# Kernel optimization log

Measured on AMD Instinct MI355X. Metric: run time of the kernel, lower is better.

The kernel has to match this reference:

```python
import jax, jax.numpy as jnp
import numpy as np

N_NODE = 2048   # nodes per graph
B = 32          # num_graphs
N = B * N_NODE  # batched node count
E = 1048576     # random edges (self loops added in reference)
C = 12          # in_channels = history window
H = 8           # attention heads
P = 9           # n_pred (out_channels)


def setup_inputs() -> dict:
    key = jax.random.key(0)
    ks = jax.random.split(key, 16)
    rn = lambda k, shp, s: jax.random.normal(k, shp, dtype=jnp.float32) * s
    return {
        "x": rn(ks[0], (N, C), 1.0),
        "edge_index": jax.random.randint(ks[1], (2, E), 0, N, dtype=jnp.int64),
        "W_gat": rn(ks[2], (C, H * C), 1.0 / np.sqrt(C)),
        "att_src": rn(ks[3], (H, C), 0.1),
        "att_dst": rn(ks[4], (H, C), 0.1),
        "bias_gat": rn(ks[5], (C,), 0.05),
        "Wih1": rn(ks[6], (4 * 32, N_NODE), 1.0 / np.sqrt(N_NODE)),
        "Whh1": rn(ks[7], (4 * 32, 32), 1.0 / np.sqrt(32)),
        "bih1": rn(ks[8], (4 * 32,), 0.05),
        "bhh1": rn(ks[9], (4 * 32,), 0.05),
        "Wih2": rn(ks[10], (4 * 128, 32), 1.0 / np.sqrt(32)),
        "Whh2": rn(ks[11], (4 * 128, 128), 1.0 / np.sqrt(128)),
        "bih2": rn(ks[12], (4 * 128,), 0.05),
        "bhh2": rn(ks[13], (4 * 128,), 0.05),
        "W_lin": rn(ks[14], (N_NODE * P, 128), 1.0 / np.sqrt(128)),
        "b_lin": rn(ks[15], (N_NODE * P,), 0.05),
    }


def _lstm(xs, Wih, Whh, bih, bhh):
    # xs: [T, B, in]; PyTorch gate order i, f, g, o
    Hh = Whh.shape[1]
    Bb = xs.shape[1]
    def step(carry, x):
        h, c = carry
        z = x @ Wih.T + h @ Whh.T + bih + bhh  # [B, 4H]
        i, f, g, o = jnp.split(z, 4, axis=-1)
        c = jax.nn.sigmoid(f) * c + jax.nn.sigmoid(i) * jnp.tanh(g)
        h = jax.nn.sigmoid(o) * jnp.tanh(c)
        return (h, c), h
    init = (jnp.zeros((Bb, Hh), xs.dtype), jnp.zeros((Bb, Hh), xs.dtype))
    _, ys = jax.lax.scan(step, init, xs)
    return ys


def reference(x, edge_index, W_gat, att_src, att_dst, bias_gat,
              Wih1, Whh1, bih1, bhh1, Wih2, Whh2, bih2, bhh2, W_lin, b_lin):
    # ---- GATConv (heads=8, concat=False, add_self_loops=True) ----
    loop = jnp.arange(N, dtype=edge_index.dtype)
    src = jnp.concatenate([edge_index[0], loop])  # message source j
    dst = jnp.concatenate([edge_index[1], loop])  # message target i
    h = (x @ W_gat).reshape(N, H, C)              # [N,H,C]
    a_s = jnp.einsum('nhc,hc->nh', h, att_src)
    a_d = jnp.einsum('nhc,hc->nh', h, att_dst)
    e = jax.nn.leaky_relu(a_s[src] + a_d[dst], 0.2)          # [E',H]
    e_max = jax.ops.segment_max(e, dst, num_segments=N)      # self loops ensure non-empty segments
    w = jnp.exp(e - e_max[dst])
    denom = jax.ops.segment_sum(w, dst, num_segments=N)
    alpha = w / denom[dst]                                   # [E',H]
    agg = jax.ops.segment_sum(alpha[:, :, None] * h[src], dst, num_segments=N)  # [N,H,C]
    g = agg.mean(axis=1) + bias_gat                          # concat=False -> head mean, [N,C]
    # (dropout is identity in eval mode)

    # ---- temporal stack ----
    seq = jnp.moveaxis(g.reshape(B, N_NODE, C), 2, 0)        # [T=C, B, N_NODE]
    h1 = _lstm(seq, Wih1, Whh1, bih1, bhh1)                  # [T,B,32]
    h2 = _lstm(h1, Wih2, Whh2, bih2, bhh2)                   # [T,B,128]
    y = h2[-1] @ W_lin.T + b_lin                             # [B, N_NODE*P]
    return y.reshape(B * N_NODE, P)
```

## Files before the change

kernel.cpp:

```cpp
#include <hip/hip_runtime.h>
#include <hip/hip_bf16.h>
#include <stdint.h>

#define NTOT 65536
#define NNODE 2048
#define CIN 12

__device__ __forceinline__ float bf2f(uint32_t u) {
    union { uint32_t i; float f; } v; v.i = u << 16; return v.f;
}
__device__ __forceinline__ uint16_t f2bf(float f) {
    union { float f; uint32_t i; } v; v.f = f;
    uint32_t x = v.i;
    uint32_t r = x + 0x7fffu + ((x >> 16) & 1u);
    return (uint16_t)(r >> 16);
}
__device__ __forceinline__ float bflo(uint32_t u) { return bf2f(u & 0xffffu); }
__device__ __forceinline__ float bfhi(uint32_t u) { return bf2f(u >> 16); }
__device__ __forceinline__ float sigmf(float x) {
    return __builtin_amdgcn_rcpf(1.0f + __expf(-x));
}
__device__ __forceinline__ float tanhfast(float x) {
    float ex = __expf(2.0f * x);
    return 1.0f - 2.0f * __builtin_amdgcn_rcpf(ex + 1.0f);
}
__device__ __forceinline__ float lrelu(float v) { return v > 0.f ? v : 0.2f * v; }

#define O_WG   16
#define O_AS   1168
#define O_AD   1264
#define O_BIAS 1360
#define O_BIH1 1376
#define O_BHH1 1504
#define O_BIH2 1632
#define O_BHH2 2144
#define O_BLIN 2656
#define O_END  21088

__device__ __forceinline__ void cvt(const void* s, float* d, int i, int bf) {
    d[i] = bf ? bf2f(((const uint16_t*)s)[i]) : ((const float*)s)[i];
}

__global__ void __launch_bounds__(256) k_pre(
    const void* x, const int* __restrict__ e32,
    const void* wg, const void* as_, const void* ad_, const void* bs,
    const void* b1, const void* bb1, const void* b2, const void* bb2,
    const void* bl, float* __restrict__ ws, int* __restrict__ deg) {
    int tid = threadIdx.x, lane = tid & 63;
    uint32_t u = ((const uint16_t*)x)[2 * lane];
    uint32_t ex = (u >> 7) & 0xFF;
    bool sane = (ex >= 0x60 && ex <= 0x9F) || (u == 0);
    unsigned long long bsx = __ballot(sane);
    bool hi_zero = (e32[2 * lane + 1] == 0);
    unsigned long long bz = __ballot(hi_zero);
    int bf = (__popcll(bsx) >= 52) ? 1 : 0;
    int st = (__popcll(bz) == 64) ? 2 : 1;
    if (blockIdx.x == 0 && tid == 0) {
        ((int*)ws)[0] = bf; ((int*)ws)[1] = st; ((int*)ws)[2] = 0;
    }
    deg[blockIdx.x * 256 + tid] = 0;
    int i = blockIdx.x * 256 + tid;
    if (i < 1152)  { cvt(wg,  ws + O_WG,   i, bf); return; } i -= 1152;
    if (i < 96)    { cvt(as_, ws + O_AS,   i, bf); return; } i -= 96;
    if (i < 96)    { cvt(ad_, ws + O_AD,   i, bf); return; } i -= 96;
    if (i < 12)    { cvt(bs,  ws + O_BIAS, i, bf); return; } i -= 12;
    if (i < 128)   { cvt(b1,  ws + O_BIH1, i, bf); return; } i -= 128;
    if (i < 128)   { cvt(bb1, ws + O_BHH1, i, bf); return; } i -= 128;
    if (i < 512)   { cvt(b2,  ws + O_BIH2, i, bf); return; } i -= 512;
    if (i < 512)   { cvt(bb2, ws + O_BHH2, i, bf); return; } i -= 512;
    if (i < 18432) { cvt(bl,  ws + O_BLIN, i, bf); }
}

__global__ void __launch_bounds__(256) k_nfa(const void* __restrict__ xraw,
                                             const float* __restrict__ Wg,
                                             const float* __restrict__ att,
                                             const int* __restrict__ flags,
                                             const int* __restrict__ e, int E,
                                             int* __restrict__ deg, int* __restrict__ rank,
                                             float* __restrict__ a_s, float* __restrict__ a_d) {
    __shared__ float sx[384];
    __shared__ float sw[1152];
    __shared__ float satt[192];
    __shared__ float sh[3072];
    int tid = threadIdx.x;
    int n0 = blockIdx.x * 32;
    if (flags[0]) {
        const uint32_t* xp = (const uint32_t*)xraw;
        for (int i = tid; i < 192; i += 256) {
            uint32_t u = xp[n0 * 6 + i];
            sx[2 * i] = bflo(u); sx[2 * i + 1] = bfhi(u);
        }
    } else {
        const float* xp = (const float*)xraw;
        for (int i = tid; i < 384; i += 256) sx[i] = xp[n0 * 12 + i];
    }
    for (int i = tid; i < 1152; i += 256) sw[i] = Wg[i];
    if (tid < 192) satt[tid] = att[tid];
    {
        long st = flags[1];
        int chunk = (E + gridDim.x - 1) / gridDim.x;
        int ebase = blockIdx.x * chunk;
        int eend = min(ebase + chunk, E);
        for (int i = ebase + tid; i < eend; i += 256) {
            int d = e[st * (E + i)];
            rank[i] = atomicAdd(&deg[d], 1);
        }
    }
    __syncthreads();
#pragma unroll
    for (int r = 0; r < 12; r++) {
        int idx = r * 256 + tid;
        int n = idx / 96, o = idx % 96;
        float acc = 0.f;
#pragma unroll
        for (int k = 0; k < 12; k++) acc += sx[n * 12 + k] * sw[k * 96 + o];
        sh[idx] = acc;
    }
    __syncthreads();
    {
        int nl = tid >> 3, h = tid & 7;
        const float* hr = sh + nl * 96 + h * 12;
        float s = 0.f, dd = 0.f;
#pragma unroll
        for (int c = 0; c < 12; c++) {
            float v = hr[c];
            s += v * satt[h * 12 + c];
            dd += v * satt[96 + h * 12 + c];
        }
        a_s[n0 * 8 + tid] = s;
        a_d[n0 * 8 + tid] = dd;
    }
}

__global__ void k_scan(const int* __restrict__ deg, int* __restrict__ offs,
                       int* __restrict__ gcount) {
    __shared__ int s[256];
    __shared__ int base;
    int t = threadIdx.x, i = blockIdx.x * 256 + t;
    int v = deg[i];
    s[t] = v; __syncthreads();
    for (int off = 1; off < 256; off <<= 1) {
        int a = (t >= off) ? s[t - off] : 0;
        __syncthreads();
        s[t] += a;
        __syncthreads();
    }
    if (t == 255) base = atomicAdd(gcount, s[255]);
    __syncthreads();
    offs[i] = base + s[t] - v;
}

__global__ void k_scatter(const int* __restrict__ e, int E, const int* __restrict__ flags,
                          const int* __restrict__ offs, const int* __restrict__ rank,
                          int* __restrict__ ssrc) {
    int i = blockIdx.x * 256 + threadIdx.x;
    if (i < E) {
        long st = flags[1];
        int s = e[st * i];
        int d = e[st * (E + i)];
        ssrc[offs[d] + rank[i]] = s;
    }
}

__global__ void __launch_bounds__(256) k_agg(
    const void* __restrict__ xraw, const float* __restrict__ WgG,
    const float* __restrict__ a_s, const float* __restrict__ a_d,
    const int* __restrict__ offs, const int* __restrict__ deg,
    const int* __restrict__ ssrc, const float* __restrict__ bias,
    const int* __restrict__ flags, float* __restrict__ gT) {
    __shared__ float swg[1152];
    __shared__ float sres[4][12];
    int tid = threadIdx.x, wave = tid >> 6, lane = tid & 63;
    for (int i = tid; i < 1152; i += 256) swg[i] = WgG[i];
    __syncthreads();
    int node = blockIdx.x * 4 + wave;
    int beg = offs[node], d = deg[node];
    int sub = lane >> 3, h = lane & 7;
    float adh = a_d[node * 8 + h];
    int bf = flags[0];
    float acc[12];
    float wsum = 0.f;
#pragma unroll
    for (int c = 0; c < 12; c++) acc[c] = 0.f;
    if (sub == 0) {
        float w = __expf(lrelu(a_s[node * 8 + h] + adh));
        wsum = w;
        if (bf) {
            const uint2* xp = (const uint2*)((const uint16_t*)xraw + node * 12);
            uint2 u0 = xp[0], u1 = xp[1], u2 = xp[2];
            acc[0] = w * bflo(u0.x); acc[1] = w * bfhi(u0.x);
            acc[2] = w * bflo(u0.y); acc[3] = w * bfhi(u0.y);
            acc[4] = w * bflo(u1.x); acc[5] = w * bfhi(u1.x);
            acc[6] = w * bflo(u1.y); acc[7] = w * bfhi(u1.y);
            acc[8] = w * bflo(u2.x); acc[9] = w * bfhi(u2.x);
            acc[10] = w * bflo(u2.y); acc[11] = w * bfhi(u2.y);
        } else {
            const float4* xp = (const float4*)((const float*)xraw + node * 12);
            float4 v0 = xp[0], v1 = xp[1], v2 = xp[2];
            acc[0] = w * v0.x; acc[1] = w * v0.y; acc[2] = w * v0.z; acc[3] = w * v0.w;
            acc[4] = w * v1.x; acc[5] = w * v1.y; acc[6] = w * v1.z; acc[7] = w * v1.w;
            acc[8] = w * v2.x; acc[9] = w * v2.y; acc[10] = w * v2.z; acc[11] = w * v2.w;
        }
    }
    for (int base = 0; base < d; base += 8) {
        int k = base + sub;
        if (k < d) {
            int s = ssrc[beg + k];
            float w = __expf(lrelu(a_s[s * 8 + h] + adh));
            wsum += w;
            if (bf) {
                const uint2* xp = (const uint2*)((const uint16_t*)xraw + s * 12);
                uint2 u0 = xp[0], u1 = xp[1], u2 = xp[2];
                acc[0] += w * bflo(u0.x); acc[1] += w * bfhi(u0.x);
                acc[2] += w * bflo(u0.y); acc[3] += w * bfhi(u0.y);
                acc[4] += w * bflo(u1.x); acc[5] += w * bfhi(u1.x);
                acc[6] += w * bflo(u1.y); acc[7] += w * bfhi(u1.y);
                acc[8] += w * bflo(u2.x); acc[9] += w * bfhi(u2.x);
                acc[10] += w * bflo(u2.y); acc[11] += w * bfhi(u2.y);
            } else {
                const float4* xp = (const float4*)((const float*)xraw + s * 12);
                float4 v0 = xp[0], v1 = xp[1], v2 = xp[2];
                acc[0] += w * v0.x; acc[1] += w * v0.y; acc[2] += w * v0.z; acc[3] += w * v0.w;
                acc[4] += w * v1.x; acc[5] += w * v1.y; acc[6] += w * v1.z; acc[7] += w * v1.w;
                acc[8] += w * v2.x; acc[9] += w * v2.y; acc[10] += w * v2.z; acc[11] += w * v2.w;
            }
        }
    }
#pragma unroll
    for (int off = 8; off <= 32; off <<= 1) {
        wsum += __shfl_xor(wsum, off, 64);
#pragma unroll
        for (int c = 0; c < 12; c++) acc[c] += __shfl_xor(acc[c], off, 64);
    }
    float invw = 1.f / wsum;
#pragma unroll
    for (int c = 0; c < 12; c++) acc[c] *= invw;
    float p0 = 0.f, p1 = 0.f;
    const float* wcol = swg + h * 12;
#pragma unroll
    for (int k = 0; k < 12; k++) {
        float a = acc[k];
        p0 += a * wcol[k * 96 + sub];
        p1 += a * wcol[k * 96 + sub + 4];
    }
#pragma unroll
    for (int off = 1; off <= 4; off <<= 1) {
        p0 += __shfl_xor(p0, off, 64);
        p1 += __shfl_xor(p1, off, 64);
    }
    if (h == 0) {
        sres[wave][sub] = p0;
        if (sub >= 4) sres[wave][sub + 4] = p1;
    }
    __syncthreads();
    if (tid < 48) {
        int no = tid / 12, c = tid % 12;
        gT[c * NTOT + blockIdx.x * 4 + no] = sres[no][c] * 0.125f + bias[c];
    }
}

__global__ void __launch_bounds__(256) k_z1(const float* __restrict__ gT,
                                            const void* __restrict__ Wraw,
                                            const float* __restrict__ b1,
                                            const float* __restrict__ b2,
                                            const int* __restrict__ flags,
                                            float* __restrict__ Z1) {
    int t = blockIdx.x >> 3, bg = (blockIdx.x & 7) * 4;
    __shared__ float sv[4][2048];
    __shared__ float zp[2][4][128];
    int tid = threadIdx.x;
#pragma unroll
    for (int q = 0; q < 4; q++)
        for (int v = tid; v < 2048; v += 256) sv[q][v] = gT[t * NTOT + (bg + q) * NNODE + v];
    __syncthreads();
    int row = tid & 127, half = tid >> 7;
    float a0 = 0.f, a1 = 0.f, a2 = 0.f, a3 = 0.f;
    int hbase = half * 1024;
    if (flags[0]) {
        const uint4* wp = (const uint4*)((const uint16_t*)Wraw + row * 2048 + hbase);
        for (int k = 0; k < 128; k++) {
            uint4 u = wp[k];
            float w0 = bflo(u.x), w1 = bfhi(u.x), w2 = bflo(u.y), w3 = bfhi(u.y);
            float w4 = bflo(u.z), w5 = bfhi(u.z), w6 = bflo(u.w), w7 = bfhi(u.w);
#pragma unroll
            for (int q = 0; q < 4; q++) {
                float4 A = *(const float4*)&sv[q][hbase + 8 * k];
                float4 B = *(const float4*)&sv[q][hbase + 8 * k + 4];
                float r = w0 * A.x + w1 * A.y + w2 * A.z + w3 * A.w
                        + w4 * B.x + w5 * B.y + w6 * B.z + w7 * B.w;
                if (q == 0) a0 += r; else if (q == 1) a1 += r;
                else if (q == 2) a2 += r; else a3 += r;
            }
        }
    } else {
        const float4* wp = (const float4*)((const float*)Wraw + row * 2048 + hbase);
        for (int k = 0; k < 256; k++) {
            float4 w = wp[k];
#pragma unroll
            for (int q = 0; q < 4; q++) {
                float4 A = *(const float4*)&sv[q][hbase + 4 * k];
                float r = w.x * A.x + w.y * A.y + w.z * A.z + w.w * A.w;
                if (q == 0) a0 += r; else if (q == 1) a1 += r;
                else if (q == 2) a2 += r; else a3 += r;
            }
        }
    }
    zp[half][0][row] = a0; zp[half][1][row] = a1;
    zp[half][2][row] = a2; zp[half][3][row] = a3;
    __syncthreads();
    if (tid < 128) {
        float bb = b1[tid] + b2[tid];
#pragma unroll
        for (int q = 0; q < 4; q++)
            Z1[t * 4096 + (bg + q) * 128 + tid] = zp[0][q][tid] + zp[1][q][tid] + bb;
    }
}

__global__ void __launch_bounds__(64) k_lstm1(
    const float* __restrict__ Z1, const void* __restrict__ Whh1r,
    const int* __restrict__ flags, float* __restrict__ h1g) {
    int b = blockIdx.x, l = threadIdx.x;
    __shared__ __align__(16) float hb1[32];
    int bf = flags[0];
    float wA[32], wB[32];
    if (bf) {
        const uint32_t* w1 = (const uint32_t*)Whh1r;
#pragma unroll
        for (int k = 0; k < 16; k++) {
            uint32_t u = w1[l * 16 + k];
            wA[2 * k] = bflo(u); wA[2 * k + 1] = bfhi(u);
            uint32_t v = w1[(l + 64) * 16 + k];
            wB[2 * k] = bflo(v); wB[2 * k + 1] = bfhi(v);
        }
    } else {
        const float* w1 = (const float*)Whh1r;
#pragma unroll
        for (int k = 0; k < 32; k++) {
            wA[k] = w1[l * 32 + k];
            wB[k] = w1[(l + 64) * 32 + k];
        }
    }
    float za[12], zg[12];
#pragma unroll
    for (int t = 0; t < 12; t++) {
        za[t] = Z1[t * 4096 + b * 128 + l];
        zg[t] = Z1[t * 4096 + b * 128 + 64 + l];
    }
    if (l < 32) hb1[l] = 0.f;
    __builtin_amdgcn_wave_barrier();
    float c = 0.f;
#pragma unroll
    for (int t = 0; t < 12; t++) {
        float d0 = za[t], d1 = zg[t];
#pragma unroll
        for (int k = 0; k < 8; k++) {
            float4 h4 = *(const float4*)&hb1[4 * k];
            d0 += wA[4*k]*h4.x + wA[4*k+1]*h4.y + wA[4*k+2]*h4.z + wA[4*k+3]*h4.w;
            d1 += wB[4*k]*h4.x + wB[4*k+1]*h4.y + wB[4*k+2]*h4.z + wB[4*k+3]*h4.w;
        }
        float e0 = __shfl_xor(d0, 32, 64);
        float e1 = __shfl_xor(d1, 32, 64);
        if (l < 32) {
            c = sigmf(e0) * c + sigmf(d0) * tanhfast(d1);
            float h = sigmf(e1) * tanhfast(c);
            hb1[l] = h;
            h1g[t * 1024 + b * 32 + l] = h;
        }
        __builtin_amdgcn_wave_barrier();
    }
}

__global__ void __launch_bounds__(512) k_wih2(
    const float* __restrict__ h1g, const void* __restrict__ Wih2r,
    const float* __restrict__ b2i, const float* __restrict__ b2h,
    const int* __restrict__ flags, float* __restrict__ z2g) {
    int tb = blockIdx.x;
    int t = tb >> 5, b = tb & 31;
    int r = threadIdx.x;
    __shared__ __align__(16) float h[32];
    if (r < 32) h[r] = h1g[t * 1024 + b * 32 + r];
    __syncthreads();
    float z = b2i[r] + b2h[r];
    const float4* hp = (const float4*)h;
    if (flags[0]) {
        const uint4* wp = (const uint4*)((const uint16_t*)Wih2r + r * 32);
#pragma unroll
        for (int k = 0; k < 4; k++) {
            uint4 u = wp[k];
            float4 h0 = hp[2 * k], h1 = hp[2 * k + 1];
            z += bflo(u.x)*h0.x + bfhi(u.x)*h0.y + bflo(u.y)*h0.z + bfhi(u.y)*h0.w
               + bflo(u.z)*h1.x + bfhi(u.z)*h1.y + bflo(u.w)*h1.z + bfhi(u.w)*h1.w;
        }
    } else {
        const float4* wp = (const float4*)((const float*)Wih2r + r * 32);
#pragma unroll
        for (int k = 0; k < 8; k++) {
            float4 w = wp[k];
            float4 h4 = hp[k];
            z += w.x*h4.x + w.y*h4.y + w.z*h4.z + w.w*h4.w;
        }
    }
    z2g[t * 16384 + b * 512 + r] = z;
}

__global__ void __launch_bounds__(512, 1) k_lstm2(
    const float* __restrict__ z2g, const void* __restrict__ Whh2r,
    const int* __restrict__ flags, float* __restrict__ h2l) {
    int b = blockIdx.x, tid = threadIdx.x;
    __shared__ __align__(16) float hb[2][128];
    int bf = flags[0];
    int lane = tid & 63, wv = tid >> 6;
    int kh = lane >> 5;
    int gp = (lane >> 4) & 1;
    int e = wv * 16 + (lane & 15);
    int rA = gp * 256 + e;
    int rB = gp * 256 + 128 + e;

    float wA[64], wB[64];
    if (bf) {
        const uint16_t* W2 = (const uint16_t*)Whh2r;
        const uint4* pA = (const uint4*)(W2 + rA * 128 + kh * 64);
        const uint4* pB = (const uint4*)(W2 + rB * 128 + kh * 64);
#pragma unroll
        for (int k = 0; k < 8; k++) {
            uint4 ua = pA[k], ub = pB[k];
            wA[8*k+0] = bflo(ua.x); wA[8*k+1] = bfhi(ua.x);
            wA[8*k+2] = bflo(ua.y); wA[8*k+3] = bfhi(ua.y);
            wA[8*k+4] = bflo(ua.z); wA[8*k+5] = bfhi(ua.z);
            wA[8*k+6] = bflo(ua.w); wA[8*k+7] = bfhi(ua.w);
            wB[8*k+0] = bflo(ub.x); wB[8*k+1] = bfhi(ub.x);
            wB[8*k+2] = bflo(ub.y); wB[8*k+3] = bfhi(ub.y);
            wB[8*k+4] = bflo(ub.z); wB[8*k+5] = bfhi(ub.z);
            wB[8*k+6] = bflo(ub.w); wB[8*k+7] = bfhi(ub.w);
        }
    } else {
        const float4* pA = (const float4*)((const float*)Whh2r + rA * 128 + kh * 64);
        const float4* pB = (const float4*)((const float*)Whh2r + rB * 128 + kh * 64);
#pragma unroll
        for (int k = 0; k < 16; k++) {
            float4 a = pA[k], c = pB[k];
            wA[4*k+0] = a.x; wA[4*k+1] = a.y; wA[4*k+2] = a.z; wA[4*k+3] = a.w;
            wB[4*k+0] = c.x; wB[4*k+1] = c.y; wB[4*k+2] = c.z; wB[4*k+3] = c.w;
        }
    }
    if (tid < 128) hb[0][tid] = 0.f;
    const float* zb = z2g + b * 512;
    float zA = 0.f, zB = 0.f;
    if (kh == 0) { zA = zb[rA]; zB = zb[rB]; }
    float c2 = 0.f;
    __syncthreads();
#pragma unroll 1
    for (int t = 0; t < 12; t++) {
        float nA = 0.f, nB = 0.f;
        if (t < 11 && kh == 0) {
            nA = zb[(t + 1) * 16384 + rA];
            nB = zb[(t + 1) * 16384 + rB];
        }
        const float4* hp = (const float4*)&hb[t & 1][kh * 64];
        float pA = zA, pB = zB;
#pragma unroll
        for (int k = 0; k < 16; k++) {
            float4 h4 = hp[k];
            pA += wA[4*k]*h4.x + wA[4*k+1]*h4.y + wA[4*k+2]*h4.z + wA[4*k+3]*h4.w;
            pB += wB[4*k]*h4.x + wB[4*k+1]*h4.y + wB[4*k+2]*h4.z + wB[4*k+3]*h4.w;
        }
        float sA = pA + __shfl_xor(pA, 32, 64);
        float sB = pB + __shfl_xor(pB, 32, 64);
        float zg_ = __shfl_xor(sA, 16, 64);
        float zo_ = __shfl_xor(sB, 16, 64);
        if (gp == 0) {
            c2 = sigmf(sB) * c2 + sigmf(sA) * tanhfast(zg_);
            float hh = sigmf(zo_) * tanhfast(c2);
            if (kh == 0) {
                hb[(t & 1) ^ 1][e] = hh;
                if (t == 11) h2l[b * 128 + e] = hh;
            }
        }
        __syncthreads();
        zA = nA; zB = nB;
    }
}

__global__ void __launch_bounds__(256) k_lin(const float* __restrict__ h2l,
                                             const void* __restrict__ Wraw,
                                             const float* __restrict__ bl,
                                             const int* __restrict__ flags,
                                             void* __restrict__ outv) {
    __shared__ float hl[8 * 128];
    int bg = blockIdx.y;
    for (int i = threadIdx.x; i < 1024; i += 256) hl[i] = h2l[bg * 1024 + i];
    __syncthreads();
    int o = blockIdx.x * 256 + threadIdx.x;
    float bb = bl[o];
    float acc[8];
#pragma unroll
    for (int b = 0; b < 8; b++) acc[b] = bb;
    int bf = flags[0];
    if (bf) {
        const uint4* wp = (const uint4*)((const uint16_t*)Wraw + o * 128);
        for (int k = 0; k < 16; k++) {
            uint4 u = wp[k];
            float w0 = bflo(u.x), w1 = bfhi(u.x), w2 = bflo(u.y), w3 = bfhi(u.y);
            float w4 = bflo(u.z), w5 = bfhi(u.z), w6 = bflo(u.w), w7 = bfhi(u.w);
#pragma unroll
            for (int b = 0; b < 8; b++) {
                const float* h8 = hl + b * 128 + k * 8;
                acc[b] += w0 * h8[0] + w1 * h8[1] + w2 * h8[2] + w3 * h8[3]
                        + w4 * h8[4] + w5 * h8[5] + w6 * h8[6] + w7 * h8[7];
            }
        }
    } else {
        const float4* wp = (const float4*)((const float*)Wraw + o * 128);
        for (int k = 0; k < 32; k++) {
            float4 w = wp[k];
#pragma unroll
            for (int b = 0; b < 8; b++) {
                const float* h4 = hl + b * 128 + k * 4;
                acc[b] += w.x * h4[0] + w.y * h4[1] + w.z * h4[2] + w.w * h4[3];
            }
        }
    }
    if (bf) {
        uint16_t* out = (uint16_t*)outv;
#pragma unroll
        for (int b = 0; b < 8; b++) out[(bg * 8 + b) * 18432 + o] = f2bf(acc[b]);
    } else {
        float* out = (float*)outv;
#pragma unroll
        for (int b = 0; b < 8; b++) out[(bg * 8 + b) * 18432 + o] = acc[b];
    }
}

extern "C" void kernel_launch(void* const* d_in, const int* in_sizes, int n_in,
                              void* d_out, int out_size, void* d_ws, size_t ws_size,
                              hipStream_t stream) {
    int E = in_sizes[1] / 2;

    float* ws = (float*)d_ws;
    int* flags = (int*)ws;
    float* cWg   = ws + O_WG;
    float* cAtt  = ws + O_AS;
    float* cBias = ws + O_BIAS;
    float* cBih1 = ws + O_BIH1;
    float* cBhh1 = ws + O_BHH1;
    float* cBih2 = ws + O_BIH2;
    float* cBhh2 = ws + O_BHH2;
    float* cBlin = ws + O_BLIN;

    float* base = ws + O_END;
    float* a_s  = base;
    float* a_d  = a_s + 524288;
    int* deg    = (int*)(a_d + 524288);
    int* offs   = deg + 65536;
    int* rank   = offs + 65536;
    int* ssrc   = rank + E;
    float* gT   = (float*)(ssrc + E);
    float* Z1   = gT + 786432;
    float* h2l  = Z1 + 49152;
    float* h1g  = h2l + 4096;
    float* z2g  = h1g + 12288;
    size_t needed = (size_t)((z2g + 196608) - ws) * 4;
    if (ws_size < needed) return;

    k_pre<<<256, 256, 0, stream>>>(d_in[0], (const int*)d_in[1],
                                   d_in[2], d_in[3], d_in[4], d_in[5],
                                   d_in[8], d_in[9], d_in[12], d_in[13], d_in[15],
                                   ws, deg);
    k_nfa<<<2048, 256, 0, stream>>>(d_in[0], cWg, cAtt, flags,
                                    (const int*)d_in[1], E, deg, rank,
                                    a_s, a_d);
    k_scan<<<256, 256, 0, stream>>>(deg, offs, flags + 2);
    k_scatter<<<(E + 255) / 256, 256, 0, stream>>>((const int*)d_in[1], E, flags,
                                                   offs, rank, ssrc);
    k_agg<<<NTOT / 4, 256, 0, stream>>>(d_in[0], cWg, a_s, a_d, offs, deg, ssrc,
                                        cBias, flags, gT);
    k_z1<<<96, 256, 0, stream>>>(gT, d_in[6], cBih1, cBhh1, flags, Z1);
    k_lstm1<<<32, 64, 0, stream>>>(Z1, d_in[7], flags, h1g);
    k_wih2<<<384, 512, 0, stream>>>(h1g, d_in[10], cBih2, cBhh2, flags, z2g);
    k_lstm2<<<32, 512, 0, stream>>>(z2g, d_in[11], flags, h2l);
    k_lin<<<dim3(72, 4), 256, 0, stream>>>(h2l, d_in[14], cBlin, flags, d_out);
}
```

Before: 316.5 us.

## Pack per-node attention scores and bf16 features into 64-byte records for gather

In the bf16 path, k_nfa now writes each node's 8 source-attention scores and its 12 bf16 input features together into one 64-byte record. k_agg gathers these records per edge instead of reading a_s and x from separate arrays. It also software-pipelines the neighbor loop by prefetching the next edge's record before computing the current one. The aim is fewer scattered cache lines per edge and hidden gather latency, at the cost of an extra 4 MB workspace buffer and more registers.

Result: faster. 307.0 us (-3.0%).

```diff
diff --git a/kernel.cpp b/kernel.cpp
--- a/kernel.cpp
+++ b/kernel.cpp
@@ -77,18 +77,22 @@
                                              const int* __restrict__ flags,
                                              const int* __restrict__ e, int E,
                                              int* __restrict__ deg, int* __restrict__ rank,
-                                             float* __restrict__ a_s, float* __restrict__ a_d) {
+                                             float* __restrict__ a_s, float* __restrict__ a_d,
+                                             float* __restrict__ rec) {
     __shared__ float sx[384];
     __shared__ float sw[1152];
     __shared__ float satt[192];
     __shared__ float sh[3072];
     int tid = threadIdx.x;
     int n0 = blockIdx.x * 32;
-    if (flags[0]) {
+    int bf = flags[0];
+    if (bf) {
         const uint32_t* xp = (const uint32_t*)xraw;
+        uint32_t* rx = (uint32_t*)rec;
         for (int i = tid; i < 192; i += 256) {
             uint32_t u = xp[n0 * 6 + i];
             sx[2 * i] = bflo(u); sx[2 * i + 1] = bfhi(u);
+            rx[(size_t)(n0 + i / 6) * 16 + 8 + i % 6] = u;
         }
     } else {
         const float* xp = (const float*)xraw;
@@ -127,7 +131,8 @@
             s += v * satt[h * 12 + c];
             dd += v * satt[96 + h * 12 + c];
         }
-        a_s[n0 * 8 + tid] = s;
+        if (bf) rec[(size_t)(n0 + nl) * 16 + h] = s;
+        else    a_s[n0 * 8 + tid] = s;
         a_d[n0 * 8 + tid] = dd;
     }
 }
@@ -167,7 +172,8 @@
     const float* __restrict__ a_s, const float* __restrict__ a_d,
     const int* __restrict__ offs, const int* __restrict__ deg,
     const int* __restrict__ ssrc, const float* __restrict__ bias,
-    const int* __restrict__ flags, float* __restrict__ gT) {
+    const int* __restrict__ flags, const float* __restrict__ rec,
+    float* __restrict__ gT) {
     __shared__ float swg[1152];
     __shared__ float sres[4][12];
     int tid = threadIdx.x, wave = tid >> 6, lane = tid & 63;
@@ -182,42 +188,63 @@
     float wsum = 0.f;
 #pragma unroll
     for (int c = 0; c < 12; c++) acc[c] = 0.f;
-    if (sub == 0) {
-        float w = __expf(lrelu(a_s[node * 8 + h] + adh));
-        wsum = w;
-        if (bf) {
-            const uint2* xp = (const uint2*)((const uint16_t*)xraw + node * 12);
-            uint2 u0 = xp[0], u1 = xp[1], u2 = xp[2];
-            acc[0] = w * bflo(u0.x); acc[1] = w * bfhi(u0.x);
-            acc[2] = w * bflo(u0.y); acc[3] = w * bfhi(u0.y);
-            acc[4] = w * bflo(u1.x); acc[5] = w * bfhi(u1.x);
-            acc[6] = w * bflo(u1.y); acc[7] = w * bfhi(u1.y);
-            acc[8] = w * bflo(u2.x); acc[9] = w * bfhi(u2.x);
-            acc[10] = w * bflo(u2.y); acc[11] = w * bfhi(u2.y);
-        } else {
+    if (bf) {
+        if (sub == 0) {
+            const float* rp0 = rec + (size_t)node * 16;
+            float asv = rp0[h];
+            float w = __expf(lrelu(asv + adh));
+            wsum = w;
+            uint4 xu = *(const uint4*)(rp0 + 8);
+            uint2 xv = *(const uint2*)(rp0 + 12);
+            acc[0] = w * bflo(xu.x); acc[1] = w * bfhi(xu.x);
+            acc[2] = w * bflo(xu.y); acc[3] = w * bfhi(xu.y);
+            acc[4] = w * bflo(xu.z); acc[5] = w * bfhi(xu.z);
+            acc[6] = w * bflo(xu.w); acc[7] = w * bfhi(xu.w);
+            acc[8] = w * bflo(xv.x); acc[9] = w * bfhi(xv.x);
+            acc[10] = w * bflo(xv.y); acc[11] = w * bfhi(xv.y);
+        }
+        if (d > 0) {
+            int k = sub;
+            int s0 = ssrc[beg + min(k, d - 1)];
+            const float* rp = rec + (size_t)s0 * 16;
+            float asv = rp[h];
+            uint4 xu = *(const uint4*)(rp + 8);
+            uint2 xv = *(const uint2*)(rp + 12);
+            for (int base = 0; base < d; base += 8, k += 8) {
+                int kn = k + 8;
+                int s1 = (kn < d) ? ssrc[beg + kn] : s0;
+                const float* rpn = rec + (size_t)s1 * 16;
+                float asv_n = rpn[h];
+                uint4 xu_n = *(const uint4*)(rpn + 8);
+                uint2 xv_n = *(const uint2*)(rpn + 12);
+                float w = __expf(lrelu(asv + adh));
+                if (k >= d) w = 0.f;
+                wsum += w;
+                acc[0] += w * bflo(xu.x); acc[1] += w * bfhi(xu.x);
+                acc[2] += w * bflo(xu.y); acc[3] += w * bfhi(xu.y);
+                acc[4] += w * bflo(xu.z); acc[5] += w * bfhi(xu.z);
+                acc[6] += w * bflo(xu.w); acc[7] += w * bfhi(xu.w);
+                acc[8] += w * bflo(xv.x); acc[9] += w * bfhi(xv.x);
+                acc[10] += w * bflo(xv.y); acc[11] += w * bfhi(xv.y);
+                asv = asv_n; xu = xu_n; xv = xv_n; s0 = s1;
+            }
+        }
+    } else {
+        if (sub == 0) {
+            float w = __expf(lrelu(a_s[node * 8 + h] + adh));
+            wsum = w;
             const float4* xp = (const float4*)((const float*)xraw + node * 12);
             float4 v0 = xp[0], v1 = xp[1], v2 = xp[2];
             acc[0] = w * v0.x; acc[1] = w * v0.y; acc[2] = w * v0.z; acc[3] = w * v0.w;
             acc[4] = w * v1.x; acc[5] = w * v1.y; acc[6] = w * v1.z; acc[7] = w * v1.w;
             acc[8] = w * v2.x; acc[9] = w * v2.y; acc[10] = w * v2.z; acc[11] = w * v2.w;
         }
-    }
-    for (int base = 0; base < d; base += 8) {
-        int k = base + sub;
-        if (k < d) {
-            int s = ssrc[beg + k];
-            float w = __expf(lrelu(a_s[s * 8 + h] + adh));
-            wsum += w;
-            if (bf) {
-                const uint2* xp = (const uint2*)((const uint16_t*)xraw + s * 12);
-                uint2 u0 = xp[0], u1 = xp[1], u2 = xp[2];
-                acc[0] += w * bflo(u0.x); acc[1] += w * bfhi(u0.x);
-                acc[2] += w * bflo(u0.y); acc[3] += w * bfhi(u0.y);
-                acc[4] += w * bflo(u1.x); acc[5] += w * bfhi(u1.x);
-                acc[6] += w * bflo(u1.y); acc[7] += w * bfhi(u1.y);
-                acc[8] += w * bflo(u2.x); acc[9] += w * bfhi(u2.x);
-                acc[10] += w * bflo(u2.y); acc[11] += w * bfhi(u2.y);
-            } else {
+        for (int base = 0; base < d; base += 8) {
+            int k = base + sub;
+            if (k < d) {
+                int s = ssrc[beg + k];
+                float w = __expf(lrelu(a_s[s * 8 + h] + adh));
+                wsum += w;
                 const float4* xp = (const float4*)((const float*)xraw + s * 12);
                 float4 v0 = xp[0], v1 = xp[1], v2 = xp[2];
                 acc[0] += w * v0.x; acc[1] += w * v0.y; acc[2] += w * v0.z; acc[3] += w * v0.w;
@@ -559,7 +586,8 @@
     float* h2l  = Z1 + 49152;
     float* h1g  = h2l + 4096;
     float* z2g  = h1g + 12288;
-    size_t needed = (size_t)((z2g + 196608) - ws) * 4;
+    float* rec  = z2g + 196608;
+    size_t needed = (size_t)((rec + 1048576) - ws) * 4;
     if (ws_size < needed) return;
 
     k_pre<<<256, 256, 0, stream>>>(d_in[0], (const int*)d_in[1],
@@ -568,12 +596,12 @@
                                    ws, deg);
     k_nfa<<<2048, 256, 0, stream>>>(d_in[0], cWg, cAtt, flags,
                                     (const int*)d_in[1], E, deg, rank,
-                                    a_s, a_d);
+                                    a_s, a_d, rec);
     k_scan<<<256, 256, 0, stream>>>(deg, offs, flags + 2);
     k_scatter<<<(E + 255) / 256, 256, 0, stream>>>((const int*)d_in[1], E, flags,
                                                    offs, rank, ssrc);
     k_agg<<<NTOT / 4, 256, 0, stream>>>(d_in[0], cWg, a_s, a_d, offs, deg, ssrc,
-                                        cBias, flags, gT);
+                                        cBias, flags, rec, gT);
     k_z1<<<96, 256, 0, stream>>>(gT, d_in[6], cBih1, cBhh1, flags, Z1);
     k_lstm1<<<32, 64, 0, stream>>>(Z1, d_in[7], flags, h1g);
     k_wih2<<<384, 512, 0, stream>>>(h1g, d_in[10], cBih2, cBhh2, flags, z2g);
```
